# Optimization experiments

Hardware: AMD Instinct MI355X
Metric: run time of the kernel (lower is better)

The kernel has to match this reference:

```python
import jax, jax.numpy as jnp
import numpy as np

B, T, N, C = 16, 12, 2048, 64
WIN = 3                    # window_size
F = 3                      # len(filters) branches
NW = T - WIN + 1           # number of windows = 10


def setup_inputs() -> dict:
    key = jax.random.key(0)
    k0, k1, k2, k3, k4 = jax.random.split(key, 5)
    data = jax.random.normal(k0, (B, T, N, C), jnp.float32)
    # scale adj so aggregated features stay O(1)
    adj = jax.random.normal(k1, (WIN * N, WIN * N), jnp.float32) / np.float32(np.sqrt(WIN * N))
    temporal_emb = jax.random.normal(k2, (1, T, 1, C), jnp.float32) * 0.1
    spatial_emb = jax.random.normal(k3, (1, 1, N, C), jnp.float32) * 0.1
    # per-window, per-filter GLU linear: C -> 2C
    W = jax.random.normal(k4, (NW, F, C, 2 * C), jnp.float32) / np.float32(np.sqrt(C))
    b = jnp.zeros((NW, F, 2 * C), jnp.float32)
    return {"data": data, "adj": adj, "temporal_emb": temporal_emb,
            "spatial_emb": spatial_emb, "W": W, "b": b}


def reference(data, adj, temporal_emb, spatial_emb, W, b):
    # data: (B,T,N,C); adj: (3N,3N)
    x = data + temporal_emb + spatial_emb                     # (B,T,N,C)
    # sliding windows of 3 time steps, flattened to 3N nodes  # (B,NW,3N,C)
    wins = jnp.stack([x[:, i:i + WIN].reshape(B, WIN * N, C) for i in range(NW)], axis=1)
    # only the middle N rows of the bmm output survive the mid-step slice,
    # so aggregate with just those rows of adj (same math, less work)
    adj_mid = adj[(WIN - 1) // 2 * N:(WIN + 1) // 2 * N]      # (N, 3N)
    agg = jnp.einsum('mn,bwnc->bwmc', adj_mid, wins)          # (B,NW,N,C)
    # per-window per-filter linear C -> 2C, then GLU
    pre = jnp.einsum('bwnc,wfcd->bwfnd', agg, W) + b[None, :, :, None, :]  # (B,NW,F,N,2C)
    lhs, rhs = jnp.split(pre, 2, axis=-1)
    glu = lhs * jax.nn.sigmoid(rhs)                           # (B,NW,F,N,C)
    # max over filter branches -> (B, T-2, N, C)
    return jnp.max(glu, axis=2)
```

## Files before the change

### kernel.cpp

```cpp
#include <hip/hip_runtime.h>
#include <hip/hip_bf16.h>

#define B_ 16
#define T_ 12
#define N_ 2048
#define C_ 64
#define NW_ 10
#define K_ 6144

#define NT32 192
#define ALDS32 4096
#define BLDS32 10240

typedef __attribute__((ext_vector_type(8))) short bf16x8;
typedef __attribute__((ext_vector_type(4))) float f32x4;

__device__ __forceinline__ unsigned short f2bf(float f) {
  union { float f; unsigned int u; } v; v.f = f;
  unsigned int u = v.u;
  return (unsigned short)((u + 0x7FFFu + ((u >> 16) & 1u)) >> 16);
}

__device__ __forceinline__ void gload16(const void* g, void* l) {
  __builtin_amdgcn_global_load_lds(
      (const __attribute__((address_space(1))) unsigned int*)g,
      (__attribute__((address_space(3))) unsigned int*)l, 16, 0, 0);
}

template<int N>
__device__ __forceinline__ void vmw() {
  if constexpr (N == 5) asm volatile("s_waitcnt vmcnt(5)" ::: "memory");
  else                  asm volatile("s_waitcnt vmcnt(0)" ::: "memory");
}

__global__ __launch_bounds__(256) void prep_all(const float* __restrict__ data,
                                                const float* __restrict__ temb,
                                                const float* __restrict__ semb,
                                                const float* __restrict__ adj,
                                                const float* __restrict__ W,
                                                unsigned short* __restrict__ xbt2,
                                                unsigned short* __restrict__ adjb3,
                                                unsigned short* __restrict__ wbt) {
  __shared__ __align__(16) unsigned short sbuf[128 * 72];
  int blk = blockIdx.x;
  int tid = threadIdx.x;
  if (blk < 6144) {
    unsigned short (*sx)[72] = (unsigned short (*)[72])sbuf;
    int nb = blk & 31;
    int bt = blk >> 5;
    int t = bt % T_;
    int n0 = nb * 64;
    const float* dbase = data + ((size_t)bt * N_ + n0) * C_;
    const float* sbase = semb + (size_t)n0 * C_;
    const float* tbase = temb + t * C_;
#pragma unroll
    for (int i = 0; i < 4; ++i) {
      int p = i * 256 + tid;
      int n = p >> 4, seg = p & 15;
      float4 dv = *(const float4*)(dbase + p * 4);
      float4 sv = *(const float4*)(sbase + p * 4);
      float4 tv = *(const float4*)(tbase + seg * 4);
      int c0 = seg * 4;
      sx[n][c0 + 0] = f2bf(dv.x + sv.x + tv.x);
      sx[n][c0 + 1] = f2bf(dv.y + sv.y + tv.y);
      sx[n][c0 + 2] = f2bf(dv.z + sv.z + tv.z);
      sx[n][c0 + 3] = f2bf(dv.w + sv.w + tv.w);
    }
    __syncthreads();
    unsigned short* obase = xbt2 + (size_t)blk * 4096;
#pragma unroll
    for (int i = 0; i < 2; ++i) {
      int q = i * 256 + tid;
      int o = q >> 6, c = q & 63;
      union { unsigned short s8[8]; uint4 v; } pk;
#pragma unroll
      for (int e = 0; e < 8; ++e) pk.s8[e] = sx[o * 8 + e][c];
      *(uint4*)(obase + (size_t)q * 8) = pk.v;
    }
  } else if (blk < 7680) {
    unsigned short (*sa)[72] = (unsigned short (*)[72])sbuf;
    int b2 = blk - 6144;
    int t = b2 % 96;
    int bmt = b2 / 96;
    const float* abase = adj + ((size_t)(N_ + bmt * 128)) * K_ + t * 64;
#pragma unroll
    for (int i = 0; i < 8; ++i) {
      int p = i * 256 + tid;
      int row = p >> 4, seg = p & 15;
      float4 v = *(const float4*)(abase + (size_t)row * K_ + seg * 4);
      int k0 = seg * 4;
      sa[row][k0 + 0] = f2bf(v.x);
      sa[row][k0 + 1] = f2bf(v.y);
      sa[row][k0 + 2] = f2bf(v.z);
      sa[row][k0 + 3] = f2bf(v.w);
    }
    __syncthreads();
    unsigned short* obase = adjb3 + (size_t)b2 * 8192;
#pragma unroll
    for (int i = 0; i < 4; ++i) {
      int g = i * 256 + tid;
      int l15 = g & 15, l4 = (g >> 4) & 3;
      int c4 = g >> 6;
      int rg = c4 & 7, KK = (c4 >> 3) & 1;
      int row = rg * 16 + l15;
      int kcol = KK * 32 + l4 * 8;
      uint4 v = *(const uint4*)&sa[row][kcol];
      *(uint4*)(obase + (size_t)g * 8) = v;
    }
  } else {
    int idx = (blk - 7680) * 256 + tid;
    int c = idx & 63;
    int d = (idx >> 6) & 127;
    int wf = idx >> 13;
    float v = W[((size_t)wf * 64 + c) * 128 + d];
    wbt[idx] = f2bf(v);
  }
}

struct SegCtx {
  const unsigned short* Asrc;
  const unsigned short* Xroot;
  int lane, wid, wid5, l4, l15, fbase;
  int bconst[5];
};

template<int UA, int UB3>
__device__ __forceinline__ void phase32(const SegCtx& s, unsigned short* ldsA,
                                        unsigned short* ldsB, int u, f32x4 (&acc)[8][5]) {
  if (u + 1 < NT32) {
    const unsigned short* As = s.Asrc + (size_t)(u + 1) * 4096;
    unsigned short* Ad = ldsA + (UA ^ 1) * ALDS32;
#pragma unroll
    for (int ci = 0; ci < 2; ++ci) {
      int rg = s.wid * 2 + ci;
      gload16(As + rg * 512 + s.lane * 8, Ad + rg * 512);
    }
  }
  if (u + 2 < NT32) {
    const unsigned short* Bs = s.Xroot + (size_t)(u + 2) * 2048;
    unsigned short* Bd = ldsB + ((UB3 + 2) % 3) * BLDS32;
#pragma unroll
    for (int ci = 0; ci < 5; ++ci) {
      int cg = s.wid5 + ci;
      gload16(Bs + s.bconst[ci], Bd + cg * 512);
    }
  }
  const unsigned short* Ab = ldsA + UA * ALDS32;
  const unsigned short* Bb = ldsB + UB3 * BLDS32;
  bf16x8 af[8], bfv[5];
#pragma unroll
  for (int c = 0; c < 5; ++c)
    bfv[c] = *(const bf16x8*)(Bb + (s.wid5 + c) * 512 + s.fbase);
#pragma unroll
  for (int i = 0; i < 8; ++i)
    af[i] = *(const bf16x8*)(Ab + i * 512 + s.fbase);
  __builtin_amdgcn_s_setprio(1);
#pragma unroll
  for (int i = 0; i < 8; ++i)
#pragma unroll
    for (int c = 0; c < 5; ++c)
      acc[i][c] = __builtin_amdgcn_mfma_f32_16x16x32_bf16(af[i], bfv[c], acc[i][c], 0, 0, 0);
  __builtin_amdgcn_s_setprio(0);
  if (u < NT32 - 2) vmw<5>();
  else if (u == NT32 - 2) vmw<0>();
  if (u < NT32 - 1) {
    __builtin_amdgcn_s_barrier();
    __builtin_amdgcn_sched_barrier(0);
  }
}

__global__ __launch_bounds__(256, 2) void gemm_agg(const unsigned short* __restrict__ adjb3,
                                                   const unsigned short* __restrict__ xbt2,
                                                   unsigned short* __restrict__ aggb) {
  __shared__ __align__(16) unsigned short ldsA[2 * ALDS32];
  __shared__ __align__(16) unsigned short ldsB[3 * BLDS32];
  int bid = blockIdx.x;
  int bmt = bid & 15;
  int bs = bid >> 4;
  int b = bs >> 1;
  int w0 = (bs & 1) * 5;
  int tid = threadIdx.x;
  SegCtx s;
  s.lane = tid & 63; s.wid = tid >> 6;
  s.wid5 = s.wid * 5;
  s.l4 = s.lane >> 4; s.l15 = s.lane & 15;
  s.fbase = s.l4 * 128 + s.l15 * 8;
  s.Asrc = adjb3 + (size_t)bmt * 786432;
  s.Xroot = xbt2 + ((size_t)(b * T_ + w0)) * C_ * N_;
  int bOffLane = s.l4 * 512 + s.l15 * 8;
#pragma unroll
  for (int ci = 0; ci < 5; ++ci) {
    int cg = s.wid5 + ci;
    s.bconst[ci] = (cg >> 2) * 131072 + (cg & 3) * 128 + bOffLane;
  }

  f32x4 acc[8][5];
#pragma unroll
  for (int i = 0; i < 8; ++i)
#pragma unroll
    for (int c = 0; c < 5; ++c) acc[i][c] = (f32x4)0.f;

  __builtin_amdgcn_sched_barrier(0);
#pragma unroll
  for (int ci = 0; ci < 2; ++ci) {
    int rg = s.wid * 2 + ci;
    gload16(s.Asrc + rg * 512 + s.lane * 8, ldsA + rg * 512);
  }
#pragma unroll
  for (int ci = 0; ci < 5; ++ci)
    gload16(s.Xroot + s.bconst[ci], ldsB + (s.wid5 + ci) * 512);
#pragma unroll
  for (int ci = 0; ci < 5; ++ci)
    gload16(s.Xroot + 2048 + s.bconst[ci], ldsB + BLDS32 + (s.wid5 + ci) * 512);
  vmw<5>();
  __builtin_amdgcn_s_barrier();
  __builtin_amdgcn_sched_barrier(0);

  for (int it = 0; it < NT32 / 6; ++it) {
    int u = it * 6;
    phase32<0, 0>(s, ldsA, ldsB, u,     acc);
    phase32<1, 1>(s, ldsA, ldsB, u + 1, acc);
    phase32<0, 2>(s, ldsA, ldsB, u + 2, acc);
    phase32<1, 0>(s, ldsA, ldsB, u + 3, acc);
    phase32<0, 1>(s, ldsA, ldsB, u + 4, acc);
    phase32<1, 2>(s, ldsA, ldsB, u + 5, acc);
  }

  unsigned short* Ob0 = aggb + (size_t)(b * NW_ + w0) * N_ * C_;
#pragma unroll
  for (int c = 0; c < 5; ++c) {
    int col = s.wid * 80 + c * 16 + s.l15;
    int g = col >> 6, cc = col & 63;
    unsigned short* Ob = Ob0 + (size_t)g * N_ * C_ + cc;
#pragma unroll
    for (int i = 0; i < 8; ++i) {
      int n0 = bmt * 128 + i * 16 + s.l4 * 4;
#pragma unroll
      for (int q = 0; q < 4; ++q)
        Ob[(size_t)(n0 + q) * C_] = f2bf(acc[i][c][q]);
    }
  }
}

__global__ __launch_bounds__(256) void glu_out(const unsigned short* __restrict__ aggb,
                                               const unsigned short* __restrict__ wbt,
                                               const float* __restrict__ bias,
                                               float* __restrict__ out) {
  __shared__ __align__(16) unsigned short sW[3 * 128 * 64];
  int bn = blockIdx.x, bw = blockIdx.y;
  int w = bw % NW_;
  int tid = threadIdx.x, lane = tid & 63, wid = tid >> 6;
  int lrow8 = lane >> 3, jl = lane & 7;
  int l15 = lane & 15, l4 = lane >> 4;
  const unsigned short* Wsrc = wbt + (size_t)w * 3 * 128 * 64;
  for (int ci = 0; ci < 12; ++ci) {
    int chunk = wid * 12 + ci;
    int row = chunk * 8 + lrow8;
    int jg = jl ^ (row & 7);
    gload16(Wsrc + (size_t)row * 64 + jg * 8, &sW[chunk * 512]);
  }
  const unsigned short* Abase = aggb + ((size_t)bw * N_ + bn * 128 + wid * 32) * C_;
  bf16x8 af[2][2];
  for (int i = 0; i < 2; ++i)
    for (int kh = 0; kh < 2; ++kh)
      af[i][kh] = *(const bf16x8*)(Abase + (size_t)(i * 16 + l15) * C_ + kh * 32 + l4 * 8);
  __syncthreads();

  float omax[2][4][4];
  for (int i = 0; i < 2; ++i)
    for (int j = 0; j < 4; ++j)
      for (int r = 0; r < 4; ++r) omax[i][j][r] = -INFINITY;

  for (int f = 0; f < 3; ++f) {
    f32x4 acc[2][8];
    for (int i = 0; i < 2; ++i)
      for (int j = 0; j < 8; ++j) acc[i][j] = (f32x4)0.f;
    for (int kh = 0; kh < 2; ++kh) {
      int gchunk = kh * 4 + l4;
      for (int j = 0; j < 8; ++j) {
        int row = f * 128 + j * 16 + l15;
        int ch = gchunk ^ (row & 7);
        bf16x8 bfr = *(const bf16x8*)&sW[row * 64 + ch * 8];
        for (int i = 0; i < 2; ++i)
          acc[i][j] = __builtin_amdgcn_mfma_f32_16x16x32_bf16(af[i][kh], bfr, acc[i][j], 0, 0, 0);
      }
    }
    for (int j = 0; j < 4; ++j) {
      float bl = bias[(w * 3 + f) * 128 + j * 16 + l15];
      float br = bias[(w * 3 + f) * 128 + 64 + j * 16 + l15];
      for (int i = 0; i < 2; ++i)
        for (int r = 0; r < 4; ++r) {
          float lhs = acc[i][j][r] + bl;
          float rhs = acc[i][j + 4][r] + br;
          float g = lhs / (1.f + __expf(-rhs));
          omax[i][j][r] = fmaxf(omax[i][j][r], g);
        }
    }
  }
  __syncthreads();
  float* tr = (float*)sW;
  float* wbase = tr + wid * 32 * 68;
#pragma unroll
  for (int i = 0; i < 2; ++i)
#pragma unroll
    for (int j = 0; j < 4; ++j)
#pragma unroll
      for (int r = 0; r < 4; ++r) {
        int row = i * 16 + l4 * 4 + r;
        int col = j * 16 + l15;
        wbase[row * 68 + col] = omax[i][j][r];
      }
  __syncthreads();
  float* Og = out + ((size_t)bw * N_ + bn * 128 + wid * 32) * C_;
#pragma unroll
  for (int it = 0; it < 8; ++it) {
    int p = it * 64 + lane;
    int row = p >> 4, seg = p & 15;
    float4 v = *(const float4*)&wbase[row * 68 + seg * 4];
    *(float4*)(Og + row * C_ + seg * 4) = v;
  }
}

extern "C" void kernel_launch(void* const* d_in, const int* in_sizes, int n_in,
                              void* d_out, int out_size, void* d_ws, size_t ws_size,
                              hipStream_t stream) {
  const float* data = (const float*)d_in[0];
  const float* adj  = (const float*)d_in[1];
  const float* temb = (const float*)d_in[2];
  const float* semb = (const float*)d_in[3];
  const float* W    = (const float*)d_in[4];
  const float* bias = (const float*)d_in[5];
  float* out = (float*)d_out;

  char* ws = (char*)d_ws;
  unsigned short* xbt2  = (unsigned short*)ws;
  unsigned short* adjb3 = (unsigned short*)(ws + 50331648);
  unsigned short* wbt   = (unsigned short*)(ws + 75497472);
  unsigned short* aggb  = (unsigned short*)(ws + 75988992);

  hipLaunchKernelGGL(prep_all, dim3(8640), dim3(256), 0, stream,
                     data, temb, semb, adj, W, xbt2, adjb3, wbt);
  hipLaunchKernelGGL(gemm_agg, dim3(512),  dim3(256), 0, stream, adjb3, xbt2, aggb);
  hipLaunchKernelGGL(glu_out,  dim3(16, 160), dim3(256), 0, stream, aggb, wbt, bias, out);
}
```

Before: 303.4 us.

## Switch aggregation GEMM to 32x32x16 MFMA with 2x2 wave tiling

The adjacency aggregation GEMM now uses 32x32x16 bf16 MFMA instructions instead of 16x16x32. Waves are arranged as a 2x2 grid, each owning a 64x160 output tile, replacing the previous layout where each wave covered all 128 rows and 80 columns. The prep kernels' packed layouts for adj and x are reordered so that LDS fragment loads stay contiguous per lane. The goal is fewer MFMA issues and fewer LDS fragment reads per unit of work. In exchange, the store epilogue scatters rows with a different pattern.

New measurement: 343.9 us. 13.4% more time.

```diff
diff --git a/kernel.cpp b/kernel.cpp
--- a/kernel.cpp
+++ b/kernel.cpp
@@ -14,6 +14,7 @@
 
 typedef __attribute__((ext_vector_type(8))) short bf16x8;
 typedef __attribute__((ext_vector_type(4))) float f32x4;
+typedef __attribute__((ext_vector_type(16))) float f32x16;
 
 __device__ __forceinline__ unsigned short f2bf(float f) {
   union { float f; unsigned int u; } v; v.f = f;
@@ -71,10 +72,14 @@
 #pragma unroll
     for (int i = 0; i < 2; ++i) {
       int q = i * 256 + tid;
-      int o = q >> 6, c = q & 63;
+      int l = q & 63;
+      int ct = (q >> 6) & 1;
+      int nb16l = q >> 7;
+      int nbase = nb16l * 16 + ((l >> 5) << 3);
+      int c = ct * 32 + (l & 31);
       union { unsigned short s8[8]; uint4 v; } pk;
 #pragma unroll
-      for (int e = 0; e < 8; ++e) pk.s8[e] = sx[o * 8 + e][c];
+      for (int e = 0; e < 8; ++e) pk.s8[e] = sx[nbase + e][c];
       *(uint4*)(obase + (size_t)q * 8) = pk.v;
     }
   } else if (blk < 7680) {
@@ -99,12 +104,13 @@
 #pragma unroll
     for (int i = 0; i < 4; ++i) {
       int g = i * 256 + tid;
-      int l15 = g & 15, l4 = (g >> 4) & 3;
-      int c4 = g >> 6;
-      int rg = c4 & 7, KK = (c4 >> 3) & 1;
-      int row = rg * 16 + l15;
-      int kcol = KK * 32 + l4 * 8;
-      uint4 v = *(const uint4*)&sa[row][kcol];
+      int l = g & 63;
+      int ch = (g >> 6) & 7;
+      int ul = g >> 9;
+      int rt = ch >> 1, ks = ch & 1;
+      int row = rt * 32 + (l & 31);
+      int kl = ul * 32 + ks * 16 + ((l >> 5) << 3);
+      uint4 v = *(const uint4*)&sa[row][kl];
       *(uint4*)(obase + (size_t)g * 8) = v;
     }
   } else {
@@ -120,20 +126,20 @@
 struct SegCtx {
   const unsigned short* Asrc;
   const unsigned short* Xroot;
-  int lane, wid, wid5, l4, l15, fbase;
+  int lane, wid, wm, wn;
   int bconst[5];
 };
 
 template<int UA, int UB3>
 __device__ __forceinline__ void phase32(const SegCtx& s, unsigned short* ldsA,
-                                        unsigned short* ldsB, int u, f32x4 (&acc)[8][5]) {
+                                        unsigned short* ldsB, int u, f32x16 (&acc)[2][5]) {
   if (u + 1 < NT32) {
     const unsigned short* As = s.Asrc + (size_t)(u + 1) * 4096;
     unsigned short* Ad = ldsA + (UA ^ 1) * ALDS32;
 #pragma unroll
     for (int ci = 0; ci < 2; ++ci) {
-      int rg = s.wid * 2 + ci;
-      gload16(As + rg * 512 + s.lane * 8, Ad + rg * 512);
+      int ch = s.wid * 2 + ci;
+      gload16(As + ch * 512 + s.lane * 8, Ad + ch * 512);
     }
   }
   if (u + 2 < NT32) {
@@ -141,25 +147,31 @@
     unsigned short* Bd = ldsB + ((UB3 + 2) % 3) * BLDS32;
 #pragma unroll
     for (int ci = 0; ci < 5; ++ci) {
-      int cg = s.wid5 + ci;
-      gload16(Bs + s.bconst[ci], Bd + cg * 512);
+      int q = s.wid * 5 + ci;
+      gload16(Bs + s.bconst[ci], Bd + q * 512);
     }
   }
   const unsigned short* Ab = ldsA + UA * ALDS32;
   const unsigned short* Bb = ldsB + UB3 * BLDS32;
-  bf16x8 af[8], bfv[5];
-#pragma unroll
-  for (int c = 0; c < 5; ++c)
-    bfv[c] = *(const bf16x8*)(Bb + (s.wid5 + c) * 512 + s.fbase);
-#pragma unroll
-  for (int i = 0; i < 8; ++i)
-    af[i] = *(const bf16x8*)(Ab + i * 512 + s.fbase);
+  bf16x8 af[2][2], bfv[5][2];
+#pragma unroll
+  for (int tc = 0; tc < 5; ++tc)
+#pragma unroll
+    for (int ks = 0; ks < 2; ++ks)
+      bfv[tc][ks] = *(const bf16x8*)(Bb + ((s.wn * 5 + tc) * 2 + ks) * 512 + s.lane * 8);
+#pragma unroll
+  for (int i = 0; i < 2; ++i)
+#pragma unroll
+    for (int ks = 0; ks < 2; ++ks)
+      af[i][ks] = *(const bf16x8*)(Ab + ((s.wm * 2 + i) * 2 + ks) * 512 + s.lane * 8);
   __builtin_amdgcn_s_setprio(1);
 #pragma unroll
-  for (int i = 0; i < 8; ++i)
-#pragma unroll
-    for (int c = 0; c < 5; ++c)
-      acc[i][c] = __builtin_amdgcn_mfma_f32_16x16x32_bf16(af[i], bfv[c], acc[i][c], 0, 0, 0);
+  for (int ks = 0; ks < 2; ++ks)
+#pragma unroll
+    for (int i = 0; i < 2; ++i)
+#pragma unroll
+      for (int tc = 0; tc < 5; ++tc)
+        acc[i][tc] = __builtin_amdgcn_mfma_f32_32x32x16_bf16(af[i][ks], bfv[tc][ks], acc[i][tc], 0, 0, 0);
   __builtin_amdgcn_s_setprio(0);
   if (u < NT32 - 2) vmw<5>();
   else if (u == NT32 - 2) vmw<0>();
@@ -182,36 +194,36 @@
   int tid = threadIdx.x;
   SegCtx s;
   s.lane = tid & 63; s.wid = tid >> 6;
-  s.wid5 = s.wid * 5;
-  s.l4 = s.lane >> 4; s.l15 = s.lane & 15;
-  s.fbase = s.l4 * 128 + s.l15 * 8;
+  s.wm = s.wid >> 1; s.wn = s.wid & 1;
   s.Asrc = adjb3 + (size_t)bmt * 786432;
   s.Xroot = xbt2 + ((size_t)(b * T_ + w0)) * C_ * N_;
-  int bOffLane = s.l4 * 512 + s.l15 * 8;
 #pragma unroll
   for (int ci = 0; ci < 5; ++ci) {
-    int cg = s.wid5 + ci;
-    s.bconst[ci] = (cg >> 2) * 131072 + (cg & 3) * 128 + bOffLane;
-  }
-
-  f32x4 acc[8][5];
-#pragma unroll
-  for (int i = 0; i < 8; ++i)
-#pragma unroll
-    for (int c = 0; c < 5; ++c) acc[i][c] = (f32x4)0.f;
+    int q = s.wid * 5 + ci;
+    int g = q >> 2;
+    int ct = (q >> 1) & 1;
+    int h = q & 1;
+    s.bconst[ci] = g * 131072 + (h * 2 + ct) * 512 + s.lane * 8;
+  }
+
+  f32x16 acc[2][5];
+#pragma unroll
+  for (int i = 0; i < 2; ++i)
+#pragma unroll
+    for (int c = 0; c < 5; ++c) acc[i][c] = (f32x16)0.f;
 
   __builtin_amdgcn_sched_barrier(0);
 #pragma unroll
   for (int ci = 0; ci < 2; ++ci) {
-    int rg = s.wid * 2 + ci;
-    gload16(s.Asrc + rg * 512 + s.lane * 8, ldsA + rg * 512);
+    int ch = s.wid * 2 + ci;
+    gload16(s.Asrc + ch * 512 + s.lane * 8, ldsA + ch * 512);
   }
 #pragma unroll
   for (int ci = 0; ci < 5; ++ci)
-    gload16(s.Xroot + s.bconst[ci], ldsB + (s.wid5 + ci) * 512);
+    gload16(s.Xroot + s.bconst[ci], ldsB + (s.wid * 5 + ci) * 512);
 #pragma unroll
   for (int ci = 0; ci < 5; ++ci)
-    gload16(s.Xroot + 2048 + s.bconst[ci], ldsB + BLDS32 + (s.wid5 + ci) * 512);
+    gload16(s.Xroot + 2048 + s.bconst[ci], ldsB + BLDS32 + (s.wid * 5 + ci) * 512);
   vmw<5>();
   __builtin_amdgcn_s_barrier();
   __builtin_amdgcn_sched_barrier(0);
@@ -227,17 +239,20 @@
   }
 
   unsigned short* Ob0 = aggb + (size_t)(b * NW_ + w0) * N_ * C_;
-#pragma unroll
-  for (int c = 0; c < 5; ++c) {
-    int col = s.wid * 80 + c * 16 + s.l15;
+  int l31 = s.lane & 31, lh = s.lane >> 5;
+#pragma unroll
+  for (int tc = 0; tc < 5; ++tc) {
+    int col = s.wn * 160 + tc * 32 + l31;
     int g = col >> 6, cc = col & 63;
     unsigned short* Ob = Ob0 + (size_t)g * N_ * C_ + cc;
 #pragma unroll
-    for (int i = 0; i < 8; ++i) {
-      int n0 = bmt * 128 + i * 16 + s.l4 * 4;
-#pragma unroll
-      for (int q = 0; q < 4; ++q)
-        Ob[(size_t)(n0 + q) * C_] = f2bf(acc[i][c][q]);
+    for (int i = 0; i < 2; ++i) {
+      int n0 = bmt * 128 + s.wm * 64 + i * 32 + lh * 4;
+#pragma unroll
+      for (int reg = 0; reg < 16; ++reg) {
+        int n = n0 + (reg & 3) + ((reg >> 2) << 3);
+        Ob[(size_t)n * C_] = f2bf(acc[i][tc][reg]);
+      }
     }
   }
 }
```
